# Kernel tuning notes

Hardware: AMD Instinct MI355X
Metric: run time of the kernel (lower is better)

Reference implementation:

```python
import jax, jax.numpy as jnp
import numpy as np
from jax import lax

INF = 1e10
R = 20          # max_distance: EDT truncated at this radius (exact under clamp)
NUM_CLASSES = 19


def _pass1d(f, axis):
    """1D squared distance transform min_{|d|<=R} (d^2 + f[shifted]), truncated.
    f: [..., H, W] with 0 at 'source' pixels, INF elsewhere. Out-of-bounds = INF
    (matches scipy, which sees nothing beyond the array border)."""
    pad = [(0, 0)] * f.ndim
    pad[axis] = (R, R)
    fp = jnp.pad(f, pad, constant_values=INF)
    n = f.shape[axis]
    out = jnp.full_like(f, INF)
    for d in range(2 * R + 1):  # fixed small loop (41 iters), jit-unrolled
        shifted = lax.slice_in_dim(fp, d, d + n, axis=axis)
        out = jnp.minimum(out, shifted + float((d - R) ** 2))
    return out


def edt_trunc(mask):
    """Euclidean distance from each True pixel to nearest False pixel,
    truncated at R (False pixels get 0). mask: [..., H, W] bool."""
    f = jnp.where(mask, INF, 0.0).astype(jnp.float32)
    g = _pass1d(f, -2)
    g = _pass1d(g, -1)
    return jnp.sqrt(jnp.minimum(g, float(R * R)))


def compute_sdf(onehot_bool):
    """Signed distance: negdist - posdist, per [B,C,H,W] one-hot masks.
    Already truncated at +-R, matching clamp(-R, R) in the torch module."""
    posdist = edt_trunc(onehot_bool)    # distance inside FG to BG
    negdist = edt_trunc(~onehot_bool)   # distance inside BG to FG
    return negdist - posdist


def setup_inputs() -> dict:
    key = jax.random.key(0)
    k1, k2 = jax.random.split(key)
    logits = jax.random.normal(k1, (8, NUM_CLASSES, 256, 512), dtype=jnp.float32)
    targets = jax.random.randint(k2, (8, 256, 512), 0, NUM_CLASSES, dtype=jnp.int64)
    return {"logits": logits, "targets": targets}


def reference(logits, targets):
    C = logits.shape[1]
    probs = jax.nn.softmax(logits, axis=1)                       # [B,C,H,W]
    onehot = jax.nn.one_hot(targets, C, axis=1, dtype=jnp.bool_)  # [B,C,H,W]
    sdf = compute_sdf(onehot)
    sdf = jnp.clip(sdf, -float(R), float(R)) / float(R)
    # mean over spatial, sum over classes, mean over batch (reduction='mean')
    per_class = jnp.mean(probs * sdf, axis=(2, 3))               # [B,C]
    loss = jnp.sum(per_class, axis=1)                            # [B]
    return jnp.mean(loss)
```

## Files before the change

kernel.cpp:

```cpp
#include <hip/hip_runtime.h>
#include <hip/hip_bf16.h>
#include <math.h>

#define NCLS 19
#define BB   8
#define HH   256
#define WW   512
#define CAP2 400u
#define SEG  8

typedef unsigned short u16x2 __attribute__((ext_vector_type(2)));

static __device__ __forceinline__ unsigned umin32(unsigned a, unsigned b) { return a < b ? a : b; }
static __device__ __forceinline__ float fsqrt_fast(float x) { return __builtin_amdgcn_sqrtf(x); }

static __device__ __forceinline__ unsigned pk_add_s(unsigned v, unsigned c) {
    unsigned d; asm("v_pk_add_u16 %0, %1, %2" : "=v"(d) : "s"(c), "v"(v)); return d;
}
static __device__ __forceinline__ unsigned pk_minv(unsigned a, unsigned b) {
    unsigned d; asm("v_pk_min_u16 %0, %1, %2" : "=v"(d) : "v"(a), "v"(b)); return d;
}
static __device__ __forceinline__ unsigned pk_maxv(unsigned a, unsigned b) {
    unsigned d; asm("v_pk_max_u16 %0, %1, %2" : "=v"(d) : "v"(a), "v"(b)); return d;
}
static __device__ __forceinline__ unsigned pk_hmin(unsigned a) {
    unsigned d;
    asm("v_pk_min_u16 %0, %1, %1 op_sel:[1,0] op_sel_hi:[0,1]" : "=v"(d) : "v"(a));
    return d;
}
static __device__ __forceinline__ void sq8(unsigned x, unsigned& w0, unsigned& w1) {
    unsigned a = x & 0x00FF00FFu;
    unsigned b = (x >> 8) & 0x00FF00FFu;
    u16x2 sa = __builtin_bit_cast(u16x2, a); sa = sa * sa;
    u16x2 sb = __builtin_bit_cast(u16x2, b); sb = sb * sb;
    unsigned ua = __builtin_bit_cast(unsigned, sa);
    unsigned ub = __builtin_bit_cast(unsigned, sb);
    w0 = __builtin_amdgcn_perm(ub, ua, 0x05040100u);
    w1 = __builtin_amdgcn_perm(ub, ua, 0x07060302u);
}

__global__ __launch_bounds__(256)
void kA_vert(const int* __restrict__ targ, unsigned char* __restrict__ vneg) {
    int gid = blockIdx.x * 256 + threadIdx.x;
    int col = gid & 4095;
    int seg = gid >> 12;
    int b = col >> 9;
    int w = col & 511;
    int h0 = seg * SEG;
    const int* tp = &targ[b * HH * WW + w];

    unsigned d[NCLS];
    unsigned pk[NCLS][2];
#pragma unroll
    for (int c = 0; c < NCLS; ++c) { d[c] = 21u; pk[c][0] = 0u; pk[c][1] = 0u; }
#pragma unroll
    for (int k = 0; k < 21 + SEG; ++k) {
        int hh = h0 - 21 + k;
        int t = -1;
        if (hh >= 0) t = tp[hh * WW];
#pragma unroll
        for (int c = 0; c < NCLS; ++c)
            d[c] = (t == c) ? 0u : d[c] + 1u;
        if (k >= 21) {
            int r = k - 21;
#pragma unroll
            for (int c = 0; c < NCLS; ++c)
                pk[c][r >> 2] |= d[c] << ((r & 3) * 8);
        }
    }
    unsigned u[NCLS];
#pragma unroll
    for (int c = 0; c < NCLS; ++c) u[c] = 21u;
#pragma unroll
    for (int k = 0; k < 21 + SEG; ++k) {
        int hh = h0 + 21 + SEG - 1 - k;
        int t = -1;
        if (hh < HH) t = tp[hh * WW];
#pragma unroll
        for (int c = 0; c < NCLS; ++c)
            u[c] = (t == c) ? 0u : u[c] + 1u;
        if (k >= 21) {
            int r = 21 + SEG - 1 - k;
#pragma unroll
            for (int c = 0; c < NCLS; ++c) {
                unsigned dv = (pk[c][r >> 2] >> ((r & 3) * 8)) & 0xffu;
                vneg[((size_t)(b * NCLS + c) * HH + hh) * WW + w] =
                    (unsigned char)umin32(dv, u[c]);
            }
        }
    }
}

__global__ __launch_bounds__(256)
void kB_main(const float* __restrict__ logits, const int* __restrict__ targ,
             const unsigned char* __restrict__ vneg,
             unsigned long long* __restrict__ acc) {
    __shared__ float wsum[4];
    int tid = threadIdx.x;
    int L = tid & 63;
    int wid = tid >> 6;
    int bh = blockIdx.x * 4 + wid;
    int b = bh >> 8;
    int h = bh & 255;

    const unsigned HALO2 = 441u | (441u << 16);

#define SQx(x) ((unsigned)((x) * (x)))
#define PK2(a, bq) (SQx(a) | (SQx(bq) << 16))
    const unsigned CE[21] = {
        PK2(-20,-19), PK2(-18,-17), PK2(-16,-15), PK2(-14,-13), PK2(-12,-11),
        PK2(-10,-9),  PK2(-8,-7),   PK2(-6,-5),   PK2(-4,-3),   PK2(-2,-1),
        PK2(0,1),     PK2(2,3),     PK2(4,5),     PK2(6,7),     PK2(8,9),
        PK2(10,11),   PK2(12,13),   PK2(14,15),   PK2(16,17),   PK2(18,19),
        PK2(20,21) };
    const unsigned CO[21] = {
        PK2(-21,-20), PK2(-19,-18), PK2(-17,-16), PK2(-15,-14), PK2(-13,-12),
        PK2(-11,-10), PK2(-9,-8),   PK2(-7,-6),   PK2(-5,-4),   PK2(-3,-2),
        PK2(-1,0),    PK2(1,2),     PK2(3,4),     PK2(5,6),     PK2(7,8),
        PK2(9,10),    PK2(11,12),   PK2(13,14),   PK2(15,16),   PK2(17,18),
        PK2(19,20) };
#undef PK2
#undef SQx

    int im1 = ((L + 63) & 63) * 4, im2 = ((L + 62) & 63) * 4, im3 = ((L + 61) & 63) * 4;
    int ip1 = ((L + 1) & 63) * 4,  ip2 = ((L + 2) & 63) * 4,  ip3 = ((L + 3) & 63) * 4;

    const uint2* vr = (const uint2*)vneg + ((size_t)(b * NCLS) * HH + h) * 64 + L;
    const float* lrow = &logits[((size_t)(b * NCLS) * HH + h) * WW + 8 * L];

    int t8[8];
    {
        const int4* tr = (const int4*)&targ[((size_t)b * HH + h) * WW + 8 * L];
        int4 ta = tr[0], tb = tr[1];
        t8[0]=ta.x; t8[1]=ta.y; t8[2]=ta.z; t8[3]=ta.w;
        t8[4]=tb.x; t8[5]=tb.y; t8[6]=tb.z; t8[7]=tb.w;
    }

    float den[8], num[8], et[8];
    unsigned m2[8];
#pragma unroll
    for (int p = 0; p < 8; ++p) { den[p]=0.f; num[p]=0.f; et[p]=0.f; m2[p]=0xFFFFu; }

    uint2 v8n = vr[0];
    float4 f0n = *(const float4*)lrow;
    float4 f1n = *(const float4*)(lrow + 4);

#pragma unroll 1
    for (int c = 0; c < NCLS; ++c) {
        uint2 v8 = v8n;
        float4 f0 = f0n, f1 = f1n;
        int cn = (c < NCLS - 1) ? c + 1 : c;
        v8n = vr[(size_t)cn * (HH * 64)];
        f0n = *(const float4*)(lrow + (size_t)cn * (HH * WW));
        f1n = *(const float4*)(lrow + (size_t)cn * (HH * WW) + 4);

        unsigned o0, o1, o2, o3;
        sq8(v8.x, o0, o1);
        sq8(v8.y, o2, o3);

        unsigned S[24];
        S[10] = o0; S[11] = o1; S[12] = o2; S[13] = o3;
        unsigned t;
        t = __builtin_amdgcn_ds_bpermute(im1, (int)o3); S[9]  = (L >= 1) ? t : HALO2;
        t = __builtin_amdgcn_ds_bpermute(im1, (int)o2); S[8]  = (L >= 1) ? t : HALO2;
        t = __builtin_amdgcn_ds_bpermute(im1, (int)o1); S[7]  = (L >= 1) ? t : HALO2;
        t = __builtin_amdgcn_ds_bpermute(im1, (int)o0); S[6]  = (L >= 1) ? t : HALO2;
        t = __builtin_amdgcn_ds_bpermute(im2, (int)o3); S[5]  = (L >= 2) ? t : HALO2;
        t = __builtin_amdgcn_ds_bpermute(im2, (int)o2); S[4]  = (L >= 2) ? t : HALO2;
        t = __builtin_amdgcn_ds_bpermute(im2, (int)o1); S[3]  = (L >= 2) ? t : HALO2;
        t = __builtin_amdgcn_ds_bpermute(im2, (int)o0); S[2]  = (L >= 2) ? t : HALO2;
        t = __builtin_amdgcn_ds_bpermute(im3, (int)o3); S[1]  = (L >= 3) ? t : HALO2;
        t = __builtin_amdgcn_ds_bpermute(im3, (int)o2); S[0]  = (L >= 3) ? t : HALO2;
        t = __builtin_amdgcn_ds_bpermute(ip1, (int)o0); S[14] = (L <= 62) ? t : HALO2;
        t = __builtin_amdgcn_ds_bpermute(ip1, (int)o1); S[15] = (L <= 62) ? t : HALO2;
        t = __builtin_amdgcn_ds_bpermute(ip1, (int)o2); S[16] = (L <= 62) ? t : HALO2;
        t = __builtin_amdgcn_ds_bpermute(ip1, (int)o3); S[17] = (L <= 62) ? t : HALO2;
        t = __builtin_amdgcn_ds_bpermute(ip2, (int)o0); S[18] = (L <= 61) ? t : HALO2;
        t = __builtin_amdgcn_ds_bpermute(ip2, (int)o1); S[19] = (L <= 61) ? t : HALO2;
        t = __builtin_amdgcn_ds_bpermute(ip2, (int)o2); S[20] = (L <= 61) ? t : HALO2;
        t = __builtin_amdgcn_ds_bpermute(ip2, (int)o3); S[21] = (L <= 61) ? t : HALO2;
        t = __builtin_amdgcn_ds_bpermute(ip3, (int)o0); S[22] = (L <= 60) ? t : HALO2;
        t = __builtin_amdgcn_ds_bpermute(ip3, (int)o1); S[23] = (L <= 60) ? t : HALO2;

        unsigned ae[4], ao[4];
#pragma unroll
        for (int r = 0; r < 4; ++r) { ae[r] = 0xFFFFFFFFu; ao[r] = 0xFFFFFFFFu; }

#pragma unroll
        for (int r = 0; r < 4; ++r)
#pragma unroll
            for (int m = 7; m <= 13; ++m) {
                ae[r] = pk_minv(ae[r], pk_add_s(S[r + m], CE[m]));
                ao[r] = pk_minv(ao[r], pk_add_s(S[r + m], CO[m]));
            }

        unsigned mx = pk_maxv(pk_maxv(pk_maxv(pk_hmin(ae[0]), pk_hmin(ao[0])),
                                      pk_maxv(pk_hmin(ae[1]), pk_hmin(ao[1]))),
                              pk_maxv(pk_maxv(pk_hmin(ae[2]), pk_hmin(ao[2])),
                                      pk_maxv(pk_hmin(ae[3]), pk_hmin(ao[3]))));
        if (!__all(mx <= (49u | (49u << 16)))) {
#pragma unroll
            for (int r = 0; r < 4; ++r) {
#pragma unroll
                for (int m = 4; m <= 6; ++m) {
                    ae[r] = pk_minv(ae[r], pk_add_s(S[r + m], CE[m]));
                    ao[r] = pk_minv(ao[r], pk_add_s(S[r + m], CO[m]));
                }
#pragma unroll
                for (int m = 14; m <= 16; ++m) {
                    ae[r] = pk_minv(ae[r], pk_add_s(S[r + m], CE[m]));
                    ao[r] = pk_minv(ao[r], pk_add_s(S[r + m], CO[m]));
                }
            }
            mx = pk_maxv(pk_maxv(pk_maxv(pk_hmin(ae[0]), pk_hmin(ao[0])),
                                 pk_maxv(pk_hmin(ae[1]), pk_hmin(ao[1]))),
                         pk_maxv(pk_maxv(pk_hmin(ae[2]), pk_hmin(ao[2])),
                                 pk_maxv(pk_hmin(ae[3]), pk_hmin(ao[3]))));
            if (!__all(mx <= (169u | (169u << 16)))) {
#pragma unroll
                for (int r = 0; r < 4; ++r) {
#pragma unroll
                    for (int m = 0; m <= 3; ++m) {
                        ae[r] = pk_minv(ae[r], pk_add_s(S[r + m], CE[m]));
                        ao[r] = pk_minv(ao[r], pk_add_s(S[r + m], CO[m]));
                    }
#pragma unroll
                    for (int m = 17; m <= 20; ++m) {
                        ae[r] = pk_minv(ae[r], pk_add_s(S[r + m], CE[m]));
                        ao[r] = pk_minv(ao[r], pk_add_s(S[r + m], CO[m]));
                    }
                }
            }
        }

        float fx[8] = {f0.x, f0.y, f0.z, f0.w, f1.x, f1.y, f1.z, f1.w};
#pragma unroll
        for (int r = 0; r < 4; ++r) {
            unsigned nd0 = pk_hmin(ae[r]) & 0xFFFFu;
            unsigned nd1 = pk_hmin(ao[r]) & 0xFFFFu;
            float e0 = __expf(fx[2 * r]), e1 = __expf(fx[2 * r + 1]);
            den[2 * r] += e0; den[2 * r + 1] += e1;
            bool is0 = (c == t8[2 * r]), is1 = (c == t8[2 * r + 1]);
            float s0 = fsqrt_fast((float)umin32(nd0, CAP2));
            float s1 = fsqrt_fast((float)umin32(nd1, CAP2));
            num[2 * r]     += is0 ? 0.f : e0 * s0;
            num[2 * r + 1] += is1 ? 0.f : e1 * s1;
            et[2 * r]     = is0 ? e0 : et[2 * r];
            et[2 * r + 1] = is1 ? e1 : et[2 * r + 1];
            m2[2 * r]     = umin32(m2[2 * r],     is0 ? 0xFFFFu : nd0);
            m2[2 * r + 1] = umin32(m2[2 * r + 1], is1 ? 0xFFFFu : nd1);
        }
    }

    float v = 0.f;
#pragma unroll
    for (int p = 0; p < 8; ++p)
        v += (num[p] - et[p] * fsqrt_fast((float)umin32(m2[p], CAP2))) / den[p];

#pragma unroll
    for (int off = 32; off >= 1; off >>= 1) v += __shfl_down(v, off);
    if (L == 0) wsum[wid] = v;
    __syncthreads();
    if (tid == 0) {
        float s = wsum[0] + wsum[1] + wsum[2] + wsum[3];
        double q = (double)s * (68719476736.0 / 20.0);
        long long iv = (long long)q;
        atomicAdd(acc, (unsigned long long)iv);
    }
}

__global__ void kC_final(const unsigned long long* __restrict__ acc,
                         float* __restrict__ out) {
    long long iv = (long long)*acc;
    double v = (double)iv / 68719476736.0;
    out[0] = (float)(v / (double)((size_t)BB * HH * WW));
}

extern "C" void kernel_launch(void* const* d_in, const int* in_sizes, int n_in,
                              void* d_out, int out_size, void* d_ws, size_t ws_size,
                              hipStream_t stream) {
    const float* logits = (const float*)d_in[0];
    const int* targ = (const int*)d_in[1];
    unsigned char* wsb = (unsigned char*)d_ws;
    unsigned long long* acc = (unsigned long long*)wsb;
    unsigned char* vneg = wsb + 64;

    (void)hipMemsetAsync(d_ws, 0, 64, stream);
    kA_vert<<<512, 256, 0, stream>>>(targ, vneg);
    kB_main<<<512, 256, 0, stream>>>(logits, targ, vneg, acc);
    kC_final<<<1, 1, 0, stream>>>(acc, (float*)d_out);
}
```

Baseline: 62.60 us.

## Split classes across waves per row and fuse final reduction via last-block

Each block now handles one image row, and its four waves each process a strided subset of the 19 classes rather than each wave walking all classes for its own row. Per-pixel partial sums are combined through shared memory before the final reduction. The memset and final kernel are removed: kA zeroes the accumulator and kB uses a last-block counter to write the output. This shortens the serial per-wave class chain and cuts launch overhead, at the cost of shared-memory traffic, an extra barrier, and a 5/4 class imbalance across waves.

```diff
diff --git a/kernel.cpp b/kernel.cpp
--- a/kernel.cpp
+++ b/kernel.cpp
@@ -40,7 +40,9 @@
 }
 
 __global__ __launch_bounds__(256)
-void kA_vert(const int* __restrict__ targ, unsigned char* __restrict__ vneg) {
+void kA_vert(const int* __restrict__ targ, unsigned char* __restrict__ vneg,
+             unsigned long long* __restrict__ acc, unsigned* __restrict__ cnt) {
+    if (blockIdx.x == 0 && threadIdx.x == 0) { *acc = 0ULL; *cnt = 0u; }
     int gid = blockIdx.x * 256 + threadIdx.x;
     int col = gid & 4095;
     int seg = gid >> 12;
@@ -94,12 +96,17 @@
 __global__ __launch_bounds__(256)
 void kB_main(const float* __restrict__ logits, const int* __restrict__ targ,
              const unsigned char* __restrict__ vneg,
-             unsigned long long* __restrict__ acc) {
+             unsigned long long* __restrict__ acc, unsigned* __restrict__ cnt,
+             float* __restrict__ out) {
+    __shared__ float sNum[4][512];
+    __shared__ float sDen[4][512];
+    __shared__ float sEt[4][512];
+    __shared__ unsigned short sM2[4][512];
     __shared__ float wsum[4];
     int tid = threadIdx.x;
     int L = tid & 63;
     int wid = tid >> 6;
-    int bh = blockIdx.x * 4 + wid;
+    int bh = blockIdx.x;
     int b = bh >> 8;
     int h = bh & 255;
 
@@ -125,8 +132,9 @@
     int im1 = ((L + 63) & 63) * 4, im2 = ((L + 62) & 63) * 4, im3 = ((L + 61) & 63) * 4;
     int ip1 = ((L + 1) & 63) * 4,  ip2 = ((L + 2) & 63) * 4,  ip3 = ((L + 3) & 63) * 4;
 
-    const uint2* vr = (const uint2*)vneg + ((size_t)(b * NCLS) * HH + h) * 64 + L;
-    const float* lrow = &logits[((size_t)(b * NCLS) * HH + h) * WW + 8 * L];
+    const uint2* vrw = (const uint2*)vneg + ((size_t)(b * NCLS + wid) * HH + h) * 64 + L;
+    const float* lroww = &logits[((size_t)(b * NCLS + wid) * HH + h) * WW + 8 * L];
+    int nc = (wid < 3) ? 5 : 4;
 
     int t8[8];
     {
@@ -141,18 +149,22 @@
 #pragma unroll
     for (int p = 0; p < 8; ++p) { den[p]=0.f; num[p]=0.f; et[p]=0.f; m2[p]=0xFFFFu; }
 
-    uint2 v8n = vr[0];
-    float4 f0n = *(const float4*)lrow;
-    float4 f1n = *(const float4*)(lrow + 4);
+    uint2 v8n = vrw[0];
+    float4 f0n = *(const float4*)lroww;
+    float4 f1n = *(const float4*)(lroww + 4);
 
 #pragma unroll 1
-    for (int c = 0; c < NCLS; ++c) {
+    for (int i = 0; i < nc; ++i) {
+        int c = wid + 4 * i;
         uint2 v8 = v8n;
         float4 f0 = f0n, f1 = f1n;
-        int cn = (c < NCLS - 1) ? c + 1 : c;
-        v8n = vr[(size_t)cn * (HH * 64)];
-        f0n = *(const float4*)(lrow + (size_t)cn * (HH * WW));
-        f1n = *(const float4*)(lrow + (size_t)cn * (HH * WW) + 4);
+        if (i + 1 < nc) {
+            size_t off = (size_t)(i + 1) * 4 * (HH * 64);
+            v8n = vrw[off];
+            const float* ln = lroww + (size_t)(i + 1) * 4 * (HH * WW);
+            f0n = *(const float4*)ln;
+            f1n = *(const float4*)(ln + 4);
+        }
 
         unsigned o0, o1, o2, o3;
         sq8(v8.x, o0, o1);
@@ -252,28 +264,58 @@
         }
     }
 
-    float v = 0.f;
-#pragma unroll
-    for (int p = 0; p < 8; ++p)
-        v += (num[p] - et[p] * fsqrt_fast((float)umin32(m2[p], CAP2))) / den[p];
+    *(float4*)&sNum[wid][8 * L]     = (float4){num[0], num[1], num[2], num[3]};
+    *(float4*)&sNum[wid][8 * L + 4] = (float4){num[4], num[5], num[6], num[7]};
+    *(float4*)&sDen[wid][8 * L]     = (float4){den[0], den[1], den[2], den[3]};
+    *(float4*)&sDen[wid][8 * L + 4] = (float4){den[4], den[5], den[6], den[7]};
+    *(float4*)&sEt[wid][8 * L]      = (float4){et[0], et[1], et[2], et[3]};
+    *(float4*)&sEt[wid][8 * L + 4]  = (float4){et[4], et[5], et[6], et[7]};
+    uint4 mq;
+    mq.x = m2[0] | (m2[1] << 16); mq.y = m2[2] | (m2[3] << 16);
+    mq.z = m2[4] | (m2[5] << 16); mq.w = m2[6] | (m2[7] << 16);
+    *(uint4*)&sM2[wid][8 * L] = mq;
+    __syncthreads();
+
+    float v;
+    {
+        int px = 2 * tid;
+        float2 n0 = *(const float2*)&sNum[0][px], n1 = *(const float2*)&sNum[1][px];
+        float2 n2 = *(const float2*)&sNum[2][px], n3 = *(const float2*)&sNum[3][px];
+        float2 d0 = *(const float2*)&sDen[0][px], d1 = *(const float2*)&sDen[1][px];
+        float2 d2 = *(const float2*)&sDen[2][px], d3 = *(const float2*)&sDen[3][px];
+        float2 e0 = *(const float2*)&sEt[0][px],  e1 = *(const float2*)&sEt[1][px];
+        float2 e2 = *(const float2*)&sEt[2][px],  e3 = *(const float2*)&sEt[3][px];
+        unsigned q0 = *(const unsigned*)&sM2[0][px], q1 = *(const unsigned*)&sM2[1][px];
+        unsigned q2 = *(const unsigned*)&sM2[2][px], q3 = *(const unsigned*)&sM2[3][px];
+        float N0 = (n0.x + n1.x) + (n2.x + n3.x);
+        float N1 = (n0.y + n1.y) + (n2.y + n3.y);
+        float D0 = (d0.x + d1.x) + (d2.x + d3.x);
+        float D1 = (d0.y + d1.y) + (d2.y + d3.y);
+        float E0 = (e0.x + e1.x) + (e2.x + e3.x);
+        float E1 = (e0.y + e1.y) + (e2.y + e3.y);
+        unsigned M0 = umin32(umin32(q0 & 0xFFFFu, q1 & 0xFFFFu),
+                             umin32(q2 & 0xFFFFu, q3 & 0xFFFFu));
+        unsigned M1 = umin32(umin32(q0 >> 16, q1 >> 16), umin32(q2 >> 16, q3 >> 16));
+        v = (N0 - E0 * fsqrt_fast((float)umin32(M0, CAP2))) / D0
+          + (N1 - E1 * fsqrt_fast((float)umin32(M1, CAP2))) / D1;
+    }
 
 #pragma unroll
     for (int off = 32; off >= 1; off >>= 1) v += __shfl_down(v, off);
-    if (L == 0) wsum[wid] = v;
+    if ((tid & 63) == 0) wsum[wid] = v;
     __syncthreads();
     if (tid == 0) {
-        float s = wsum[0] + wsum[1] + wsum[2] + wsum[3];
+        float s = (wsum[0] + wsum[1]) + (wsum[2] + wsum[3]);
         double q = (double)s * (68719476736.0 / 20.0);
-        long long iv = (long long)q;
-        atomicAdd(acc, (unsigned long long)iv);
-    }
-}
-
-__global__ void kC_final(const unsigned long long* __restrict__ acc,
-                         float* __restrict__ out) {
-    long long iv = (long long)*acc;
-    double v = (double)iv / 68719476736.0;
-    out[0] = (float)(v / (double)((size_t)BB * HH * WW));
+        atomicAdd(acc, (unsigned long long)(long long)q);
+        __threadfence();
+        unsigned prev = atomicAdd(cnt, 1u);
+        if (prev == gridDim.x - 1) {
+            unsigned long long tot = atomicAdd(acc, 0ULL);
+            double vv = (double)(long long)tot / 68719476736.0;
+            out[0] = (float)(vv / (double)((size_t)BB * HH * WW));
+        }
+    }
 }
 
 extern "C" void kernel_launch(void* const* d_in, const int* in_sizes, int n_in,
@@ -283,10 +325,10 @@
     const int* targ = (const int*)d_in[1];
     unsigned char* wsb = (unsigned char*)d_ws;
     unsigned long long* acc = (unsigned long long*)wsb;
+    unsigned* cnt = (unsigned*)(wsb + 8);
     unsigned char* vneg = wsb + 64;
 
-    (void)hipMemsetAsync(d_ws, 0, 64, stream);
-    kA_vert<<<512, 256, 0, stream>>>(targ, vneg);
-    kB_main<<<512, 256, 0, stream>>>(logits, targ, vneg, acc);
-    kC_final<<<1, 1, 0, stream>>>(acc, (float*)d_out);
-}
+    kA_vert<<<512, 256, 0, stream>>>(targ, vneg, acc, cnt);
+    kB_main<<<BB * HH, 256, 0, stream>>>(logits, targ, vneg, acc, cnt,
+                                         (float*)d_out);
+}
```

Measured after the change: 104.7 us. +67.2%, slower.
